# Kernel tuning notes

Measured on AMD Instinct MI355X. Metric: run time of the kernel, lower is better.

Reference implementation:

```python
import jax, jax.numpy as jnp
import numpy as np

WIN = 7
N = WIN * WIN            # 49 tokens per window
HEADS = 6
C = 192
NW = 4096                # windows per image
B_ = 8192                # batch * num_windows
EPS = 1e-12              # F.normalize eps


def _make_relative_position_index():
    # mirrors the torch buffer construction (torch.meshgrid default = 'ij')
    coords = np.stack(np.meshgrid(np.arange(WIN), np.arange(WIN), indexing='ij'))  # [2,7,7]
    flat = coords.reshape(2, -1)                                # [2,49]
    rel = flat[:, :, None] - flat[:, None, :]                   # [2,49,49]
    rel = rel.transpose(1, 2, 0).astype(np.int64)               # [49,49,2]
    rel[..., 0] += WIN - 1
    rel[..., 1] += WIN - 1
    rel[..., 0] *= 2 * WIN - 1
    return rel.sum(-1)                                          # [49,49], values in [0, 169)


def setup_inputs() -> dict:
    key = jax.random.key(0)
    ks = jax.random.split(key, 8)
    x = jax.random.normal(ks[0], (B_, N, C), dtype=jnp.float32)
    mask = jnp.zeros((NW, N, N), dtype=jnp.float32)
    d_l = jax.random.uniform(ks[1], (B_,), dtype=jnp.float32)
    w = 0.02
    Wq = jax.random.normal(ks[2], (C, C), dtype=jnp.float32) * w
    Wk = jax.random.normal(ks[3], (C, C), dtype=jnp.float32) * w
    Wv = jax.random.normal(ks[4], (C, C), dtype=jnp.float32) * w
    Wp = jax.random.normal(ks[5], (C, C), dtype=jnp.float32) * w
    temperature = jnp.ones((HEADS, 1, 1), dtype=jnp.float32)
    rpb_table = jax.random.normal(ks[6], ((2 * WIN - 1) ** 2, HEADS), dtype=jnp.float32) * w
    rel_index = jnp.asarray(_make_relative_position_index(), dtype=jnp.int32)
    return {"x": x, "mask": mask, "d_l": d_l, "Wq": Wq, "Wk": Wk, "Wv": Wv,
            "Wp": Wp, "temperature": temperature, "rpb_table": rpb_table,
            "rel_index": rel_index}


def _l2norm(t):
    # F.normalize(dim=-1): t / max(||t||_2, eps)
    n = jnp.sqrt(jnp.sum(t * t, axis=-1, keepdims=True))
    return t / jnp.maximum(n, EPS)


def reference(x, mask, d_l, Wq, Wk, Wv, Wp, temperature, rpb_table, rel_index):
    b, n, c = x.shape
    hd = c // HEADS  # head dim = 32

    def split_heads(t):
        return t.reshape(b, n, HEADS, hd).transpose(0, 2, 1, 3)  # b h n d

    q = split_heads(x @ Wq.T)
    k = split_heads(x @ Wk.T)
    v = split_heads(x @ Wv.T)

    q = _l2norm(q)
    k = _l2norm(k)

    attn = jnp.einsum('bhnd,bhmd->bhnm', q, k) * temperature  # temperature [h,1,1] broadcasts

    bias = rpb_table[rel_index.reshape(-1)].reshape(n, n, HEADS)  # gather [49,49,h]
    attn = attn + bias.transpose(2, 0, 1)[None]                   # [1,h,n,n]

    nW = mask.shape[0]
    attn = attn.reshape(b // nW, nW, HEADS, n, n) + mask[None, :, None]
    attn = attn.reshape(b, HEADS, n, n)

    attn = attn * d_l[:, None, None, None]  # degrade-level modulation
    attn = jax.nn.softmax(attn, axis=-1)

    out = jnp.einsum('bhnm,bhmd->bhnd', attn, v)
    out = out.transpose(0, 2, 1, 3).reshape(b, n, c)
    return out @ Wp.T
```

## Files before the change

### kernel.cpp

```cpp
#include <hip/hip_runtime.h>

#define NTOK 49
#define HEADS 6
#define CDIM 192
#define NWIN 4096

typedef unsigned short u16;
typedef unsigned int u32;
typedef unsigned long long u64;
typedef __attribute__((ext_vector_type(8))) __bf16 bf16x8;
typedef __attribute__((ext_vector_type(4))) float floatx4;

#define OFF_X 0
#define OFF_Q 25600
#define OFF_K 51200
#define OFF_V 76800
#define OFF_P 104448
#define LDS_BYTES 122880

__device__ __forceinline__ u16 f2bf(float f) {
  union { float f; u32 u; } v; v.f = f;
  u32 u = v.u;
  u = (u + 0x7FFFu + ((u >> 16) & 1u)) >> 16;
  return (u16)u;
}
__device__ __forceinline__ float bf2f(u16 u) {
  union { u32 u; float f; } v; v.u = ((u32)u) << 16;
  return v.f;
}
__device__ __forceinline__ void st4bf(u16* p, float a, float b, float c, float d) {
  u64 t = (u64)f2bf(a) | ((u64)f2bf(b) << 16) | ((u64)f2bf(c) << 32) | ((u64)f2bf(d) << 48);
  *(u64*)p = t;
}

__global__ __launch_bounds__(256)
void wprep(const float* __restrict__ Wq, const float* __restrict__ Wk,
           const float* __restrict__ Wv, const float* __restrict__ Wp,
           const float* __restrict__ rpb, const int* __restrict__ rel,
           u16* __restrict__ w_bf, float* __restrict__ bias) {
  const int tid = blockIdx.x * blockDim.x + threadIdx.x;
  const int stride = gridDim.x * blockDim.x;
  for (int i = tid; i < 4 * CDIM * CDIM; i += stride) {
    const int p = i / (CDIM * CDIM), e = i % (CDIM * CDIM);
    float v = (p == 0) ? Wq[e] : (p == 1) ? Wk[e] : (p == 2) ? Wv[e] : Wp[e];
    w_bf[i] = f2bf(v);
  }
  for (int i = tid; i < HEADS * NTOK * NTOK; i += stride) {
    const int h = i / (NTOK * NTOK), nm = i % (NTOK * NTOK);
    bias[i] = rpb[rel[nm] * HEADS + h];
  }
}

__global__ __launch_bounds__(512, 2)
void wattn_main(const float* __restrict__ x, const float* __restrict__ mask,
                const float* __restrict__ d_l, const float* __restrict__ temp,
                const u16* __restrict__ w_bf, const float* __restrict__ bias,
                float* __restrict__ out) {
  extern __shared__ __align__(16) char smem[];
  u16* Xb = (u16*)(smem + OFF_X);
  u16* Qn = (u16*)(smem + OFF_Q);
  u16* Kn = (u16*)(smem + OFF_K);
  u16* Vt = (u16*)(smem + OFF_V);
  u16* Pw = (u16*)(smem + OFF_P);

  const int b = blockIdx.x;
  const int tid = threadIdx.x;
  const int wave = tid >> 6;
  const int lane = tid & 63;
  const int g = lane >> 4;
  const int nl = lane & 15;

  {
    const float* xb = x + (size_t)b * (NTOK * CDIM);
    for (int i = tid; i < NTOK * CDIM / 4; i += 512) {
      const int n = i / 48;
      const int c = (i - n * 48) * 4;
      const float4 v = *(const float4*)(xb + n * CDIM + c);
      st4bf(Xb + n * 200 + c, v.x, v.y, v.z, v.w);
    }
    for (int i = tid; i < 15 * 48; i += 512) {
      const int n = 49 + i / 48;
      const int c = (i % 48) * 4;
      *(u64*)(Xb + n * 200 + c) = 0ull;
    }
  }
  __syncthreads();

  {
    bf16x8 xf[4][6];
#pragma unroll
    for (int nt = 0; nt < 4; ++nt)
#pragma unroll
      for (int k = 0; k < 6; ++k)
        xf[nt][k] = *(const bf16x8*)(Xb + (nt * 16 + nl) * 200 + k * 32 + g * 8);

    for (int u = wave; u < 36; u += 8) {
      const int p = u / 12, o = u % 12;
      const u16* wb = w_bf + p * (CDIM * CDIM) + (o * 16 + nl) * CDIM + g * 8;
      bf16x8 wf[6];
#pragma unroll
      for (int k = 0; k < 6; ++k) wf[k] = *(const bf16x8*)(wb + k * 32);
      floatx4 acc[4];
#pragma unroll
      for (int nt = 0; nt < 4; ++nt) acc[nt] = (floatx4){0.f, 0.f, 0.f, 0.f};
      if (p < 2) {
#pragma unroll
        for (int k = 0; k < 6; ++k)
#pragma unroll
          for (int nt = 0; nt < 4; ++nt)
            acc[nt] = __builtin_amdgcn_mfma_f32_16x16x32_bf16(wf[k], xf[nt][k], acc[nt], 0, 0, 0);
        u16* dst = (p == 0 ? Qn : Kn);
#pragma unroll
        for (int nt = 0; nt < 4; ++nt)
          st4bf(dst + (nt * 16 + nl) * 200 + o * 16 + g * 4,
                acc[nt][0], acc[nt][1], acc[nt][2], acc[nt][3]);
      } else {
#pragma unroll
        for (int k = 0; k < 6; ++k)
#pragma unroll
          for (int nt = 0; nt < 4; ++nt)
            acc[nt] = __builtin_amdgcn_mfma_f32_16x16x32_bf16(xf[nt][k], wf[k], acc[nt], 0, 0, 0);
#pragma unroll
        for (int nt = 0; nt < 4; ++nt)
          st4bf(Vt + (o * 16 + nl) * 72 + nt * 16 + g * 4,
                acc[nt][0], acc[nt][1], acc[nt][2], acc[nt][3]);
      }
    }
  }
  __syncthreads();

  {
    const int sub = tid & 3;
    for (int ru = tid >> 2; ru < 2 * HEADS * NTOK; ru += 128) {
      const int t = ru / (HEADS * NTOK);
      const int rem = ru - t * (HEADS * NTOK);
      const int h = rem / NTOK, n = rem - h * NTOK;
      u16* base = (t == 0 ? Qn : Kn) + n * 200 + h * 32 + sub * 8;
      u64 lo = *(u64*)base;
      u64 hi = *(u64*)(base + 4);
      float f[8];
#pragma unroll
      for (int e = 0; e < 4; ++e) f[e] = bf2f((u16)(lo >> (16 * e)));
#pragma unroll
      for (int e = 0; e < 4; ++e) f[4 + e] = bf2f((u16)(hi >> (16 * e)));
      float ss = 0.f;
#pragma unroll
      for (int e = 0; e < 8; ++e) ss += f[e] * f[e];
      ss += __shfl_xor(ss, 1);
      ss += __shfl_xor(ss, 2);
      const float inv = 1.0f / fmaxf(sqrtf(ss), 1e-12f);
      st4bf(base, f[0] * inv, f[1] * inv, f[2] * inv, f[3] * inv);
      st4bf(base + 4, f[4] * inv, f[5] * inv, f[6] * inv, f[7] * inv);
    }
  }
  __syncthreads();

  {
    const float dl = d_l[b];
    const int wmask = b & (NWIN - 1);
    u16* Pb = Pw + wave * (16 * 72);
    for (int t = wave; t < 24; t += 8) {
      const int h = t >> 2, nt2 = t & 3;
      const int n = nt2 * 16 + nl;
      const int ncl = n < 49 ? n : 48;
      const float tdl = temp[h] * dl;
      const bf16x8 qf = *(const bf16x8*)(Qn + n * 200 + h * 32 + g * 8);
      floatx4 sacc[4];
#pragma unroll
      for (int rt = 0; rt < 4; ++rt) {
        const bf16x8 kf = *(const bf16x8*)(Kn + (rt * 16 + nl) * 200 + h * 32 + g * 8);
        sacc[rt] = __builtin_amdgcn_mfma_f32_16x16x32_bf16(kf, qf, (floatx4){0.f, 0.f, 0.f, 0.f}, 0, 0, 0);
      }
      const float* brow = bias + (h * NTOK + ncl) * NTOK;
      const float* mrow = mask + ((size_t)wmask * NTOK + ncl) * NTOK;
      float L[4][4];
      float pmax = -1e30f;
#pragma unroll
      for (int rt = 0; rt < 4; ++rt)
#pragma unroll
        for (int r = 0; r < 4; ++r) {
          const int m = rt * 16 + g * 4 + r;
          const int mcl = m < 49 ? m : 48;
          const float bm = (brow[mcl] + mrow[mcl]) * dl;
          float lv = fmaf(sacc[rt][r], tdl, bm);
          lv = (m < 49) ? lv : -1e30f;
          L[rt][r] = lv;
          pmax = fmaxf(pmax, lv);
        }
      pmax = fmaxf(pmax, __shfl_xor(pmax, 16));
      pmax = fmaxf(pmax, __shfl_xor(pmax, 32));
      float psum = 0.f;
#pragma unroll
      for (int rt = 0; rt < 4; ++rt)
#pragma unroll
        for (int r = 0; r < 4; ++r) {
          const int m = rt * 16 + g * 4 + r;
          const float e = (m < 49) ? __expf(L[rt][r] - pmax) : 0.f;
          L[rt][r] = e;
          psum += e;
        }
      psum += __shfl_xor(psum, 16);
      psum += __shfl_xor(psum, 32);
      const float rinv = 1.0f / psum;
#pragma unroll
      for (int rt = 0; rt < 4; ++rt)
        st4bf(Pb + nl * 72 + rt * 16 + g * 4,
              L[rt][0] * rinv, L[rt][1] * rinv, L[rt][2] * rinv, L[rt][3] * rinv);
      floatx4 oacc[2];
      oacc[0] = (floatx4){0.f, 0.f, 0.f, 0.f};
      oacc[1] = (floatx4){0.f, 0.f, 0.f, 0.f};
#pragma unroll
      for (int ks = 0; ks < 2; ++ks) {
        const bf16x8 pf = *(const bf16x8*)(Pb + nl * 72 + ks * 32 + g * 8);
#pragma unroll
        for (int dt = 0; dt < 2; ++dt) {
          const bf16x8 vf = *(const bf16x8*)(Vt + (h * 32 + dt * 16 + nl) * 72 + ks * 32 + g * 8);
          oacc[dt] = __builtin_amdgcn_mfma_f32_16x16x32_bf16(vf, pf, oacc[dt], 0, 0, 0);
        }
      }
#pragma unroll
      for (int dt = 0; dt < 2; ++dt)
        st4bf(Xb + n * 200 + h * 32 + dt * 16 + g * 4,
              oacc[dt][0], oacc[dt][1], oacc[dt][2], oacc[dt][3]);
    }
  }
  __syncthreads();

  {
    bf16x8 af[4][6];
#pragma unroll
    for (int nt = 0; nt < 4; ++nt)
#pragma unroll
      for (int k = 0; k < 6; ++k)
        af[nt][k] = *(const bf16x8*)(Xb + (nt * 16 + nl) * 200 + k * 32 + g * 8);
    float* outb = out + (size_t)b * (NTOK * CDIM);
    const u16* wpb = w_bf + 3 * (CDIM * CDIM);
    for (int o = wave; o < 12; o += 8) {
      const u16* wb = wpb + (o * 16 + nl) * CDIM + g * 8;
      bf16x8 wf[6];
#pragma unroll
      for (int k = 0; k < 6; ++k) wf[k] = *(const bf16x8*)(wb + k * 32);
      floatx4 acc[4];
#pragma unroll
      for (int nt = 0; nt < 4; ++nt) acc[nt] = (floatx4){0.f, 0.f, 0.f, 0.f};
#pragma unroll
      for (int k = 0; k < 6; ++k)
#pragma unroll
        for (int nt = 0; nt < 4; ++nt)
          acc[nt] = __builtin_amdgcn_mfma_f32_16x16x32_bf16(wf[k], af[nt][k], acc[nt], 0, 0, 0);
#pragma unroll
      for (int nt = 0; nt < 4; ++nt) {
        const int n = nt * 16 + nl;
        if (n < 49) {
          float4 v;
          v.x = acc[nt][0]; v.y = acc[nt][1]; v.z = acc[nt][2]; v.w = acc[nt][3];
          *(float4*)(outb + n * CDIM + o * 16 + g * 4) = v;
        }
      }
    }
  }
}

extern "C" void kernel_launch(void* const* d_in, const int* in_sizes, int n_in,
                              void* d_out, int out_size, void* d_ws, size_t ws_size,
                              hipStream_t stream) {
  const float* x    = (const float*)d_in[0];
  const float* mask = (const float*)d_in[1];
  const float* dl   = (const float*)d_in[2];
  const float* Wq   = (const float*)d_in[3];
  const float* Wk   = (const float*)d_in[4];
  const float* Wv   = (const float*)d_in[5];
  const float* Wp   = (const float*)d_in[6];
  const float* temp = (const float*)d_in[7];
  const float* rpb  = (const float*)d_in[8];
  const int*   rel  = (const int*)d_in[9];

  u16* w_bf = (u16*)d_ws;
  float* bias = (float*)((char*)d_ws + (size_t)4 * CDIM * CDIM * sizeof(u16));
  float* o = (float*)d_out;

  (void)hipFuncSetAttribute((const void*)wattn_main,
                            hipFuncAttributeMaxDynamicSharedMemorySize, LDS_BYTES);

  wprep<<<256, 256, 0, stream>>>(Wq, Wk, Wv, Wp, rpb, rel, w_bf, bias);
  wattn_main<<<8192, 512, LDS_BYTES, stream>>>(x, mask, dl, temp, w_bf, bias, o);
}
```

Before: 646.9 us.

## Shrink LDS footprint via buffer aliasing and register-resident P to raise occupancy

The change reduces LDS from about 120KB to 75KB by aliasing X with V^T and Q with the attention output. It keeps softmax probabilities in registers, using cross-lane shuffles instead of an LDS round trip, and swizzles the V^T layout to avoid bank conflicts. The QKV projection is split so each wave pair handles half the tokens, and the output projection is re-tiled. Launch bounds go to 4 blocks per CU so more windows are resident. In exchange it adds an extra barrier, more shuffles, register pressure from the 4-block bound, and scalar (uncoalesced) final output stores.

Result: slower. 841.2 us (+30.0%).

```diff
diff --git a/kernel.cpp b/kernel.cpp
--- a/kernel.cpp
+++ b/kernel.cpp
@@ -10,13 +10,14 @@
 typedef unsigned long long u64;
 typedef __attribute__((ext_vector_type(8))) __bf16 bf16x8;
 typedef __attribute__((ext_vector_type(4))) float floatx4;
-
-#define OFF_X 0
-#define OFF_Q 25600
-#define OFF_K 51200
-#define OFF_V 76800
-#define OFF_P 104448
-#define LDS_BYTES 122880
+typedef __attribute__((ext_vector_type(4))) u32 u32x4;
+
+struct __attribute__((aligned(4))) F4 { float f[4]; };
+
+#define R1_OFF 0
+#define R2_OFF 25600
+#define R3_OFF 51200
+#define LDS_BYTES 76800
 
 __device__ __forceinline__ u16 f2bf(float f) {
   union { float f; u32 u; } v; v.f = f;
@@ -24,13 +25,20 @@
   u = (u + 0x7FFFu + ((u >> 16) & 1u)) >> 16;
   return (u16)u;
 }
+__device__ __forceinline__ void st4bf(u16* p, float a, float b, float c, float d) {
+  u64 t = (u64)f2bf(a) | ((u64)f2bf(b) << 16) | ((u64)f2bf(c) << 32) | ((u64)f2bf(d) << 48);
+  *(u64*)p = t;
+}
 __device__ __forceinline__ float bf2f(u16 u) {
   union { u32 u; float f; } v; v.u = ((u32)u) << 16;
   return v.f;
 }
-__device__ __forceinline__ void st4bf(u16* p, float a, float b, float c, float d) {
-  u64 t = (u64)f2bf(a) | ((u64)f2bf(b) << 16) | ((u64)f2bf(c) << 32) | ((u64)f2bf(d) << 48);
-  *(u64*)p = t;
+__device__ __forceinline__ u32 pack2bf(float lo, float hi) {
+  return (u32)f2bf(lo) | ((u32)f2bf(hi) << 16);
+}
+__device__ __forceinline__ bf16x8 frag_from_words(u32 a, u32 b, u32 c, u32 d) {
+  u32x4 t = {a, b, c, d};
+  return __builtin_bit_cast(bf16x8, t);
 }
 
 __global__ __launch_bounds__(256)
@@ -51,17 +59,17 @@
   }
 }
 
-__global__ __launch_bounds__(512, 2)
+__global__ __launch_bounds__(512, 4)
 void wattn_main(const float* __restrict__ x, const float* __restrict__ mask,
                 const float* __restrict__ d_l, const float* __restrict__ temp,
                 const u16* __restrict__ w_bf, const float* __restrict__ bias,
                 float* __restrict__ out) {
   extern __shared__ __align__(16) char smem[];
-  u16* Xb = (u16*)(smem + OFF_X);
-  u16* Qn = (u16*)(smem + OFF_Q);
-  u16* Kn = (u16*)(smem + OFF_K);
-  u16* Vt = (u16*)(smem + OFF_V);
-  u16* Pw = (u16*)(smem + OFF_P);
+  u16* Xs  = (u16*)(smem + R1_OFF);
+  u16* Vt  = (u16*)(smem + R1_OFF);
+  u16* Qn  = (u16*)(smem + R2_OFF);
+  u16* AOB = (u16*)(smem + R2_OFF);
+  u16* Kn  = (u16*)(smem + R3_OFF);
 
   const int b = blockIdx.x;
   const int tid = threadIdx.x;
@@ -72,58 +80,62 @@
 
   {
     const float* xb = x + (size_t)b * (NTOK * CDIM);
-    for (int i = tid; i < NTOK * CDIM / 4; i += 512) {
+    for (int i = tid; i < NTOK * 48; i += 512) {
       const int n = i / 48;
       const int c = (i - n * 48) * 4;
       const float4 v = *(const float4*)(xb + n * CDIM + c);
-      st4bf(Xb + n * 200 + c, v.x, v.y, v.z, v.w);
+      st4bf(Xs + n * 200 + c, v.x, v.y, v.z, v.w);
     }
     for (int i = tid; i < 15 * 48; i += 512) {
-      const int n = 49 + i / 48;
+      const int n = NTOK + i / 48;
       const int c = (i % 48) * 4;
-      *(u64*)(Xb + n * 200 + c) = 0ull;
-    }
-  }
-  __syncthreads();
-
-  {
-    bf16x8 xf[4][6];
-#pragma unroll
-    for (int nt = 0; nt < 4; ++nt)
+      *(u64*)(Xs + n * 200 + c) = 0ull;
+    }
+  }
+  __syncthreads();
+
+  const int nthalf = wave & 1;
+  const int wg = wave >> 1;
+  bf16x8 xf[2][6];
+#pragma unroll
+  for (int nt2 = 0; nt2 < 2; ++nt2)
+#pragma unroll
+    for (int k = 0; k < 6; ++k)
+      xf[nt2][k] = *(const bf16x8*)(Xs + (nthalf * 32 + nt2 * 16 + nl) * 200 + k * 32 + g * 8);
+  __syncthreads();
+
+  for (int t = wg; t < 36; t += 4) {
+    const int p = t / 12, o = t % 12;
+    const u16* wb = w_bf + p * (CDIM * CDIM) + (o * 16 + nl) * CDIM + g * 8;
+    bf16x8 wf[6];
+#pragma unroll
+    for (int k = 0; k < 6; ++k) wf[k] = *(const bf16x8*)(wb + k * 32);
+    floatx4 acc[2];
+    acc[0] = (floatx4){0.f, 0.f, 0.f, 0.f};
+    acc[1] = (floatx4){0.f, 0.f, 0.f, 0.f};
+    if (p < 2) {
 #pragma unroll
       for (int k = 0; k < 6; ++k)
-        xf[nt][k] = *(const bf16x8*)(Xb + (nt * 16 + nl) * 200 + k * 32 + g * 8);
-
-    for (int u = wave; u < 36; u += 8) {
-      const int p = u / 12, o = u % 12;
-      const u16* wb = w_bf + p * (CDIM * CDIM) + (o * 16 + nl) * CDIM + g * 8;
-      bf16x8 wf[6];
-#pragma unroll
-      for (int k = 0; k < 6; ++k) wf[k] = *(const bf16x8*)(wb + k * 32);
-      floatx4 acc[4];
-#pragma unroll
-      for (int nt = 0; nt < 4; ++nt) acc[nt] = (floatx4){0.f, 0.f, 0.f, 0.f};
-      if (p < 2) {
-#pragma unroll
-        for (int k = 0; k < 6; ++k)
-#pragma unroll
-          for (int nt = 0; nt < 4; ++nt)
-            acc[nt] = __builtin_amdgcn_mfma_f32_16x16x32_bf16(wf[k], xf[nt][k], acc[nt], 0, 0, 0);
-        u16* dst = (p == 0 ? Qn : Kn);
-#pragma unroll
-        for (int nt = 0; nt < 4; ++nt)
-          st4bf(dst + (nt * 16 + nl) * 200 + o * 16 + g * 4,
-                acc[nt][0], acc[nt][1], acc[nt][2], acc[nt][3]);
-      } else {
-#pragma unroll
-        for (int k = 0; k < 6; ++k)
-#pragma unroll
-          for (int nt = 0; nt < 4; ++nt)
-            acc[nt] = __builtin_amdgcn_mfma_f32_16x16x32_bf16(xf[nt][k], wf[k], acc[nt], 0, 0, 0);
-#pragma unroll
-        for (int nt = 0; nt < 4; ++nt)
-          st4bf(Vt + (o * 16 + nl) * 72 + nt * 16 + g * 4,
-                acc[nt][0], acc[nt][1], acc[nt][2], acc[nt][3]);
+#pragma unroll
+        for (int nt2 = 0; nt2 < 2; ++nt2)
+          acc[nt2] = __builtin_amdgcn_mfma_f32_16x16x32_bf16(wf[k], xf[nt2][k], acc[nt2], 0, 0, 0);
+      u16* dst = (p == 0 ? Qn : Kn);
+#pragma unroll
+      for (int nt2 = 0; nt2 < 2; ++nt2)
+        st4bf(dst + (nthalf * 32 + nt2 * 16 + nl) * 200 + o * 16 + g * 4,
+              acc[nt2][0], acc[nt2][1], acc[nt2][2], acc[nt2][3]);
+    } else {
+#pragma unroll
+      for (int k = 0; k < 6; ++k)
+#pragma unroll
+        for (int nt2 = 0; nt2 < 2; ++nt2)
+          acc[nt2] = __builtin_amdgcn_mfma_f32_16x16x32_bf16(xf[nt2][k], wf[k], acc[nt2], 0, 0, 0);
+      const int row = o * 16 + nl;
+#pragma unroll
+      for (int nt2 = 0; nt2 < 2; ++nt2) {
+        const int col = nthalf * 32 + nt2 * 16 + g * 4;
+        const int colS = (col + ((nl & 3) << 4)) & 63;
+        st4bf(Vt + row * 64 + colS, acc[nt2][0], acc[nt2][1], acc[nt2][2], acc[nt2][3]);
       }
     }
   }
@@ -155,107 +167,138 @@
   }
   __syncthreads();
 
+  const float dl = d_l[b];
+  const int wmask = b & (NWIN - 1);
+  const int srcA = nl + ((lane & 16) << 1);
+  const int srcB = srcA + 16;
+  const bool hi = (g >> 1) != 0;
+  u32 pf[3][2][4];
+#pragma unroll
+  for (int i = 0; i < 3; ++i) {
+    const int t = wave + 8 * i;
+    const int h = t >> 2, nt = t & 3;
+    const int n = nt * 16 + nl;
+    const int ncl = n < NTOK ? n : NTOK - 1;
+    const float tdl = temp[h] * dl;
+    const bf16x8 qf = *(const bf16x8*)(Qn + n * 200 + h * 32 + g * 8);
+    floatx4 sacc[4];
+#pragma unroll
+    for (int rt = 0; rt < 4; ++rt) {
+      const bf16x8 kf = *(const bf16x8*)(Kn + (rt * 16 + nl) * 200 + h * 32 + g * 8);
+      sacc[rt] = __builtin_amdgcn_mfma_f32_16x16x32_bf16(kf, qf, (floatx4){0.f, 0.f, 0.f, 0.f}, 0, 0, 0);
+    }
+    const float* brow = bias + (h * NTOK + ncl) * NTOK;
+    const float* mrow = mask + ((size_t)wmask * NTOK + ncl) * NTOK;
+    float L[4][4];
+    float pmax = -1e30f;
+#pragma unroll
+    for (int rt = 0; rt < 3; ++rt) {
+      const F4 b4 = *(const F4*)(brow + rt * 16 + g * 4);
+      const F4 m4 = *(const F4*)(mrow + rt * 16 + g * 4);
+#pragma unroll
+      for (int r = 0; r < 4; ++r) {
+        const float lv = fmaf(sacc[rt][r], tdl, (b4.f[r] + m4.f[r]) * dl);
+        L[rt][r] = lv;
+        pmax = fmaxf(pmax, lv);
+      }
+    }
+    {
+      const float lv48 = fmaf(sacc[3][0], tdl, (brow[48] + mrow[48]) * dl);
+#pragma unroll
+      for (int r = 0; r < 4; ++r) L[3][r] = -1e30f;
+      if (g == 0) { L[3][0] = lv48; pmax = fmaxf(pmax, lv48); }
+    }
+    pmax = fmaxf(pmax, __shfl_xor(pmax, 16));
+    pmax = fmaxf(pmax, __shfl_xor(pmax, 32));
+    float psum = 0.f;
+#pragma unroll
+    for (int rt = 0; rt < 4; ++rt)
+#pragma unroll
+      for (int r = 0; r < 4; ++r) {
+        const float e = __expf(L[rt][r] - pmax);
+        L[rt][r] = e;
+        psum += e;
+      }
+    psum += __shfl_xor(psum, 16);
+    psum += __shfl_xor(psum, 32);
+    const float rinv = 1.0f / psum;
+    u32 pk[4][2];
+#pragma unroll
+    for (int rt = 0; rt < 4; ++rt)
+#pragma unroll
+      for (int w2 = 0; w2 < 2; ++w2)
+        pk[rt][w2] = pack2bf(L[rt][2 * w2] * rinv, L[rt][2 * w2 + 1] * rinv);
+#pragma unroll
+    for (int ks = 0; ks < 2; ++ks) {
+      const u32 a0 = __shfl((int)pk[2 * ks][0], srcA), b0 = __shfl((int)pk[2 * ks + 1][0], srcA);
+      const u32 a1 = __shfl((int)pk[2 * ks][1], srcA), b1 = __shfl((int)pk[2 * ks + 1][1], srcA);
+      const u32 a2 = __shfl((int)pk[2 * ks][0], srcB), b2 = __shfl((int)pk[2 * ks + 1][0], srcB);
+      const u32 a3 = __shfl((int)pk[2 * ks][1], srcB), b3 = __shfl((int)pk[2 * ks + 1][1], srcB);
+      pf[i][ks][0] = hi ? b0 : a0;
+      pf[i][ks][1] = hi ? b1 : a1;
+      pf[i][ks][2] = hi ? b2 : a2;
+      pf[i][ks][3] = hi ? b3 : a3;
+    }
+  }
+  __syncthreads();
+
+#pragma unroll
+  for (int i = 0; i < 3; ++i) {
+    const int t = wave + 8 * i;
+    const int h = t >> 2, nt = t & 3;
+    floatx4 oacc[2];
+    oacc[0] = (floatx4){0.f, 0.f, 0.f, 0.f};
+    oacc[1] = (floatx4){0.f, 0.f, 0.f, 0.f};
+#pragma unroll
+    for (int ks = 0; ks < 2; ++ks) {
+      const bf16x8 pfr = frag_from_words(pf[i][ks][0], pf[i][ks][1], pf[i][ks][2], pf[i][ks][3]);
+#pragma unroll
+      for (int dt = 0; dt < 2; ++dt) {
+        const int row = h * 32 + dt * 16 + nl;
+        const int colS = (ks * 32 + g * 8 + ((nl & 3) << 4)) & 63;
+        const bf16x8 vf = *(const bf16x8*)(Vt + row * 64 + colS);
+        oacc[dt] = __builtin_amdgcn_mfma_f32_16x16x32_bf16(vf, pfr, oacc[dt], 0, 0, 0);
+      }
+    }
+    u32 pka[2][2];
+#pragma unroll
+    for (int dt = 0; dt < 2; ++dt)
+#pragma unroll
+      for (int w2 = 0; w2 < 2; ++w2)
+        pka[dt][w2] = pack2bf(oacc[dt][2 * w2], oacc[dt][2 * w2 + 1]);
+    const u32 a0 = __shfl((int)pka[0][0], srcA), b0 = __shfl((int)pka[1][0], srcA);
+    const u32 a1 = __shfl((int)pka[0][1], srcA), b1 = __shfl((int)pka[1][1], srcA);
+    const u32 a2 = __shfl((int)pka[0][0], srcB), b2 = __shfl((int)pka[1][0], srcB);
+    const u32 a3 = __shfl((int)pka[0][1], srcB), b3 = __shfl((int)pka[1][1], srcB);
+    u32x4 frag;
+    frag[0] = hi ? b0 : a0;
+    frag[1] = hi ? b1 : a1;
+    frag[2] = hi ? b2 : a2;
+    frag[3] = hi ? b3 : a3;
+    *(u32x4*)(AOB + ((size_t)(nt * 6 + h) * 64 + lane) * 8) = frag;
+  }
+  __syncthreads();
+
   {
-    const float dl = d_l[b];
-    const int wmask = b & (NWIN - 1);
-    u16* Pb = Pw + wave * (16 * 72);
-    for (int t = wave; t < 24; t += 8) {
-      const int h = t >> 2, nt2 = t & 3;
-      const int n = nt2 * 16 + nl;
-      const int ncl = n < 49 ? n : 48;
-      const float tdl = temp[h] * dl;
-      const bf16x8 qf = *(const bf16x8*)(Qn + n * 200 + h * 32 + g * 8);
-      floatx4 sacc[4];
-#pragma unroll
-      for (int rt = 0; rt < 4; ++rt) {
-        const bf16x8 kf = *(const bf16x8*)(Kn + (rt * 16 + nl) * 200 + h * 32 + g * 8);
-        sacc[rt] = __builtin_amdgcn_mfma_f32_16x16x32_bf16(kf, qf, (floatx4){0.f, 0.f, 0.f, 0.f}, 0, 0, 0);
-      }
-      const float* brow = bias + (h * NTOK + ncl) * NTOK;
-      const float* mrow = mask + ((size_t)wmask * NTOK + ncl) * NTOK;
-      float L[4][4];
-      float pmax = -1e30f;
-#pragma unroll
-      for (int rt = 0; rt < 4; ++rt)
-#pragma unroll
-        for (int r = 0; r < 4; ++r) {
-          const int m = rt * 16 + g * 4 + r;
-          const int mcl = m < 49 ? m : 48;
-          const float bm = (brow[mcl] + mrow[mcl]) * dl;
-          float lv = fmaf(sacc[rt][r], tdl, bm);
-          lv = (m < 49) ? lv : -1e30f;
-          L[rt][r] = lv;
-          pmax = fmaxf(pmax, lv);
-        }
-      pmax = fmaxf(pmax, __shfl_xor(pmax, 16));
-      pmax = fmaxf(pmax, __shfl_xor(pmax, 32));
-      float psum = 0.f;
-#pragma unroll
-      for (int rt = 0; rt < 4; ++rt)
-#pragma unroll
-        for (int r = 0; r < 4; ++r) {
-          const int m = rt * 16 + g * 4 + r;
-          const float e = (m < 49) ? __expf(L[rt][r] - pmax) : 0.f;
-          L[rt][r] = e;
-          psum += e;
-        }
-      psum += __shfl_xor(psum, 16);
-      psum += __shfl_xor(psum, 32);
-      const float rinv = 1.0f / psum;
-#pragma unroll
-      for (int rt = 0; rt < 4; ++rt)
-        st4bf(Pb + nl * 72 + rt * 16 + g * 4,
-              L[rt][0] * rinv, L[rt][1] * rinv, L[rt][2] * rinv, L[rt][3] * rinv);
-      floatx4 oacc[2];
-      oacc[0] = (floatx4){0.f, 0.f, 0.f, 0.f};
-      oacc[1] = (floatx4){0.f, 0.f, 0.f, 0.f};
-#pragma unroll
-      for (int ks = 0; ks < 2; ++ks) {
-        const bf16x8 pf = *(const bf16x8*)(Pb + nl * 72 + ks * 32 + g * 8);
-#pragma unroll
-        for (int dt = 0; dt < 2; ++dt) {
-          const bf16x8 vf = *(const bf16x8*)(Vt + (h * 32 + dt * 16 + nl) * 72 + ks * 32 + g * 8);
-          oacc[dt] = __builtin_amdgcn_mfma_f32_16x16x32_bf16(vf, pf, oacc[dt], 0, 0, 0);
-        }
-      }
-#pragma unroll
-      for (int dt = 0; dt < 2; ++dt)
-        st4bf(Xb + n * 200 + h * 32 + dt * 16 + g * 4,
-              oacc[dt][0], oacc[dt][1], oacc[dt][2], oacc[dt][3]);
-    }
-  }
-  __syncthreads();
-
-  {
-    bf16x8 af[4][6];
-#pragma unroll
-    for (int nt = 0; nt < 4; ++nt)
-#pragma unroll
-      for (int k = 0; k < 6; ++k)
-        af[nt][k] = *(const bf16x8*)(Xb + (nt * 16 + nl) * 200 + k * 32 + g * 8);
     float* outb = out + (size_t)b * (NTOK * CDIM);
     const u16* wpb = w_bf + 3 * (CDIM * CDIM);
-    for (int o = wave; o < 12; o += 8) {
-      const u16* wb = wpb + (o * 16 + nl) * CDIM + g * 8;
-      bf16x8 wf[6];
-#pragma unroll
-      for (int k = 0; k < 6; ++k) wf[k] = *(const bf16x8*)(wb + k * 32);
-      floatx4 acc[4];
-#pragma unroll
-      for (int nt = 0; nt < 4; ++nt) acc[nt] = (floatx4){0.f, 0.f, 0.f, 0.f};
-#pragma unroll
-      for (int k = 0; k < 6; ++k)
-#pragma unroll
-        for (int nt = 0; nt < 4; ++nt)
-          acc[nt] = __builtin_amdgcn_mfma_f32_16x16x32_bf16(wf[k], af[nt][k], acc[nt], 0, 0, 0);
-#pragma unroll
-      for (int nt = 0; nt < 4; ++nt) {
-        const int n = nt * 16 + nl;
-        if (n < 49) {
-          float4 v;
-          v.x = acc[nt][0]; v.y = acc[nt][1]; v.z = acc[nt][2]; v.w = acc[nt][3];
-          *(float4*)(outb + n * CDIM + o * 16 + g * 4) = v;
-        }
+    for (int t = wave; t < 48; t += 8) {
+      const int o = t >> 2, nt = t & 3;
+      bf16x8 af[6], wfp[6];
+#pragma unroll
+      for (int h = 0; h < 6; ++h)
+        af[h] = *(const bf16x8*)(AOB + ((nt * 6 + h) * 64 + lane) * 8);
+#pragma unroll
+      for (int ks = 0; ks < 6; ++ks)
+        wfp[ks] = *(const bf16x8*)(wpb + (o * 16 + nl) * CDIM + ks * 32 + g * 8);
+      floatx4 acc = (floatx4){0.f, 0.f, 0.f, 0.f};
+#pragma unroll
+      for (int ks = 0; ks < 6; ++ks)
+        acc = __builtin_amdgcn_mfma_f32_16x16x32_bf16(af[ks], wfp[ks], acc, 0, 0, 0);
+#pragma unroll
+      for (int r = 0; r < 4; ++r) {
+        const int tok = nt * 16 + g * 4 + r;
+        if (tok < NTOK) outb[tok * CDIM + o * 16 + nl] = acc[r];
       }
     }
   }
```

## Split fused window attention into QKV-projection and attention kernels via workspace

Applied to the files above, without the earlier changes.

Replaces the single large-LDS fused kernel with two kernels. The first projects Q, K and V into bf16 global buffers, keeping x fragments in registers. The second does the normalization, softmax, PV and output projection using small LDS, so more blocks fit per CU. This aims to remove the occupancy limit from 120KB of LDS, but costs a global round trip of about 150MB of intermediates. If the workspace is too small it falls back to the old fused kernel.

Result: slower. 1.004 ms (+55.2%).

```diff
diff --git a/kernel.cpp b/kernel.cpp
--- a/kernel.cpp
+++ b/kernel.cpp
@@ -10,13 +10,9 @@
 typedef unsigned long long u64;
 typedef __attribute__((ext_vector_type(8))) __bf16 bf16x8;
 typedef __attribute__((ext_vector_type(4))) float floatx4;
-
-#define OFF_X 0
-#define OFF_Q 25600
-#define OFF_K 51200
-#define OFF_V 76800
-#define OFF_P 104448
-#define LDS_BYTES 122880
+typedef __attribute__((ext_vector_type(4))) u32 u32x4;
+
+struct __attribute__((aligned(4))) F4 { float f[4]; };
 
 __device__ __forceinline__ u16 f2bf(float f) {
   union { float f; u32 u; } v; v.f = f;
@@ -24,13 +20,24 @@
   u = (u + 0x7FFFu + ((u >> 16) & 1u)) >> 16;
   return (u16)u;
 }
+__device__ __forceinline__ void st4bf(u16* p, float a, float b, float c, float d) {
+  u64 t = (u64)f2bf(a) | ((u64)f2bf(b) << 16) | ((u64)f2bf(c) << 32) | ((u64)f2bf(d) << 48);
+  *(u64*)p = t;
+}
 __device__ __forceinline__ float bf2f(u16 u) {
   union { u32 u; float f; } v; v.u = ((u32)u) << 16;
   return v.f;
 }
-__device__ __forceinline__ void st4bf(u16* p, float a, float b, float c, float d) {
-  u64 t = (u64)f2bf(a) | ((u64)f2bf(b) << 16) | ((u64)f2bf(c) << 32) | ((u64)f2bf(d) << 48);
-  *(u64*)p = t;
+__device__ __forceinline__ float bflo(u32 u) {
+  union { u32 u; float f; } v; v.u = u << 16;
+  return v.f;
+}
+__device__ __forceinline__ float bfhi(u32 u) {
+  union { u32 u; float f; } v; v.u = u & 0xffff0000u;
+  return v.f;
+}
+__device__ __forceinline__ u32 pack2bf(float lo, float hi) {
+  return (u32)f2bf(lo) | ((u32)f2bf(hi) << 16);
 }
 
 __global__ __launch_bounds__(256)
@@ -51,17 +58,230 @@
   }
 }
 
+__global__ __launch_bounds__(256, 3)
+void k1_qkv(const float* __restrict__ x, const u16* __restrict__ w_bf,
+            u16* __restrict__ Qg, u16* __restrict__ Kg, u16* __restrict__ Vt) {
+  const int w = blockIdx.x;
+  const int wave = threadIdx.x >> 6;
+  const int lane = threadIdx.x & 63;
+  const int g = lane >> 4, nl = lane & 15;
+  const float* xw = x + (size_t)w * (NTOK * CDIM);
+
+  bf16x8 xf[4][6];
+#pragma unroll
+  for (int nt = 0; nt < 4; ++nt) {
+    const int tok = nt * 16 + nl;
+#pragma unroll
+    for (int k = 0; k < 6; ++k) {
+      if (tok < NTOK) {
+        const float4 lo = *(const float4*)(xw + tok * CDIM + k * 32 + g * 8);
+        const float4 hi = *(const float4*)(xw + tok * CDIM + k * 32 + g * 8 + 4);
+        u32x4 t;
+        t[0] = pack2bf(lo.x, lo.y); t[1] = pack2bf(lo.z, lo.w);
+        t[2] = pack2bf(hi.x, hi.y); t[3] = pack2bf(hi.z, hi.w);
+        xf[nt][k] = __builtin_bit_cast(bf16x8, t);
+      } else {
+        u32x4 t = {0u, 0u, 0u, 0u};
+        xf[nt][k] = __builtin_bit_cast(bf16x8, t);
+      }
+    }
+  }
+
+  for (int t = wave; t < 36; t += 4) {
+    const int p = t / 12, c = t % 12;
+    const u16* wb = w_bf + p * (CDIM * CDIM) + (c * 16 + nl) * CDIM + g * 8;
+    bf16x8 wf[6];
+#pragma unroll
+    for (int k = 0; k < 6; ++k) wf[k] = *(const bf16x8*)(wb + k * 32);
+    floatx4 acc[4];
+#pragma unroll
+    for (int nt = 0; nt < 4; ++nt) acc[nt] = (floatx4){0.f, 0.f, 0.f, 0.f};
+    if (p < 2) {
+#pragma unroll
+      for (int k = 0; k < 6; ++k)
+#pragma unroll
+        for (int nt = 0; nt < 4; ++nt)
+          acc[nt] = __builtin_amdgcn_mfma_f32_16x16x32_bf16(wf[k], xf[nt][k], acc[nt], 0, 0, 0);
+      const int h = c >> 1, half = c & 1;
+      u16* dst = (p == 0 ? Qg : Kg) + (size_t)(w * 6 + h) * (NTOK * 32);
+#pragma unroll
+      for (int nt = 0; nt < 4; ++nt) {
+        const int tok = nt * 16 + nl;
+        if (tok < NTOK)
+          st4bf(dst + tok * 32 + half * 16 + g * 4,
+                acc[nt][0], acc[nt][1], acc[nt][2], acc[nt][3]);
+      }
+    } else {
+#pragma unroll
+      for (int k = 0; k < 6; ++k)
+#pragma unroll
+        for (int nt = 0; nt < 4; ++nt)
+          acc[nt] = __builtin_amdgcn_mfma_f32_16x16x32_bf16(xf[nt][k], wf[k], acc[nt], 0, 0, 0);
+      u16* dst = Vt + ((size_t)w * CDIM + c * 16 + nl) * 64;
+#pragma unroll
+      for (int nt = 0; nt < 4; ++nt)
+        st4bf(dst + nt * 16 + g * 4, acc[nt][0], acc[nt][1], acc[nt][2], acc[nt][3]);
+    }
+  }
+}
+
+#define K2_LDS (25600 + 13824 + 3072)
+__global__ __launch_bounds__(384, 4)
+void k2_attn(const u16* __restrict__ Qg, const u16* __restrict__ Kg,
+             const u16* __restrict__ Vt, const float* __restrict__ mask,
+             const float* __restrict__ d_l, const float* __restrict__ temp,
+             const float* __restrict__ bias, const u16* __restrict__ w_bf,
+             float* __restrict__ out) {
+  extern __shared__ __align__(16) char smem[];
+  u16* AO = (u16*)smem;
+  u16* Pall = (u16*)(smem + 25600);
+  float* nrm = (float*)(smem + 25600 + 13824);
+
+  const int w = blockIdx.x;
+  const int h = threadIdx.x >> 6;
+  const int lane = threadIdx.x & 63;
+  const int g = lane >> 4, nl = lane & 15;
+  const float dl = d_l[w];
+  const float tdl = temp[h] * dl;
+  const size_t qkbase = (size_t)(w * 6 + h) * (NTOK * 32);
+
+  {
+    const u16* krow = Kg + qkbase + lane * 32;
+    const u16* qrow = Qg + qkbase + lane * 32;
+    float ssk = 0.f, ssq = 0.f;
+#pragma unroll
+    for (int q4 = 0; q4 < 4; ++q4) {
+      const u32x4 kk = *(const u32x4*)(krow + q4 * 8);
+      const u32x4 qq = *(const u32x4*)(qrow + q4 * 8);
+#pragma unroll
+      for (int e = 0; e < 4; ++e) {
+        const float k0 = bflo(kk[e]), k1 = bfhi(kk[e]);
+        const float q0 = bflo(qq[e]), q1 = bfhi(qq[e]);
+        ssk = fmaf(k0, k0, fmaf(k1, k1, ssk));
+        ssq = fmaf(q0, q0, fmaf(q1, q1, ssq));
+      }
+    }
+    nrm[h * 128 + lane] = 1.f / fmaxf(sqrtf(ssk), 1e-12f);
+    nrm[h * 128 + 64 + lane] = 1.f / fmaxf(sqrtf(ssq), 1e-12f);
+  }
+
+  u16* Pb = Pall + h * (16 * 72);
+  bf16x8 kf[4];
+#pragma unroll
+  for (int rt = 0; rt < 4; ++rt)
+    kf[rt] = *(const bf16x8*)(Kg + qkbase + (rt * 16 + nl) * 32 + g * 8);
+  const int wm = w & (NWIN - 1);
+
+  for (int nt = 0; nt < 4; ++nt) {
+    const int n = nt * 16 + nl;
+    const int ncl = n < NTOK ? n : NTOK - 1;
+    const bf16x8 qf = *(const bf16x8*)(Qg + qkbase + n * 32 + g * 8);
+    floatx4 sacc[4];
+#pragma unroll
+    for (int rt = 0; rt < 4; ++rt)
+      sacc[rt] = __builtin_amdgcn_mfma_f32_16x16x32_bf16(kf[rt], qf, (floatx4){0.f, 0.f, 0.f, 0.f}, 0, 0, 0);
+    const float qr = nrm[h * 128 + 64 + n] * tdl;
+    const float* brow = bias + (h * NTOK + ncl) * NTOK;
+    const float* mrow = mask + ((size_t)wm * NTOK + ncl) * NTOK;
+    float L[4][4];
+    float pmax = -1e30f;
+#pragma unroll
+    for (int rt = 0; rt < 3; ++rt) {
+      const F4 b4 = *(const F4*)(brow + rt * 16 + g * 4);
+      const F4 m4 = *(const F4*)(mrow + rt * 16 + g * 4);
+      const F4 kr = *(const F4*)(nrm + h * 128 + rt * 16 + g * 4);
+#pragma unroll
+      for (int r = 0; r < 4; ++r) {
+        const float lv = fmaf(sacc[rt][r] * kr.f[r], qr, (b4.f[r] + m4.f[r]) * dl);
+        L[rt][r] = lv;
+        pmax = fmaxf(pmax, lv);
+      }
+    }
+    {
+      const float lv48 = fmaf(sacc[3][0] * nrm[h * 128 + 48], qr, (brow[48] + mrow[48]) * dl);
+      L[3][0] = L[3][1] = L[3][2] = L[3][3] = -1e30f;
+      if (g == 0) { L[3][0] = lv48; pmax = fmaxf(pmax, lv48); }
+    }
+    pmax = fmaxf(pmax, __shfl_xor(pmax, 16));
+    pmax = fmaxf(pmax, __shfl_xor(pmax, 32));
+    float psum = 0.f;
+#pragma unroll
+    for (int rt = 0; rt < 4; ++rt)
+#pragma unroll
+      for (int r = 0; r < 4; ++r) {
+        const float e = __expf(L[rt][r] - pmax);
+        L[rt][r] = e;
+        psum += e;
+      }
+    psum += __shfl_xor(psum, 16);
+    psum += __shfl_xor(psum, 32);
+    const float rinv = 1.0f / psum;
+#pragma unroll
+    for (int rt = 0; rt < 4; ++rt)
+      st4bf(Pb + nl * 72 + rt * 16 + g * 4,
+            L[rt][0] * rinv, L[rt][1] * rinv, L[rt][2] * rinv, L[rt][3] * rinv);
+    floatx4 oacc[2];
+    oacc[0] = (floatx4){0.f, 0.f, 0.f, 0.f};
+    oacc[1] = (floatx4){0.f, 0.f, 0.f, 0.f};
+#pragma unroll
+    for (int ks = 0; ks < 2; ++ks) {
+      const bf16x8 pfr = *(const bf16x8*)(Pb + nl * 72 + ks * 32 + g * 8);
+#pragma unroll
+      for (int dt = 0; dt < 2; ++dt) {
+        const bf16x8 vf = *(const bf16x8*)(Vt + ((size_t)w * CDIM + h * 32 + dt * 16 + nl) * 64 + ks * 32 + g * 8);
+        oacc[dt] = __builtin_amdgcn_mfma_f32_16x16x32_bf16(vf, pfr, oacc[dt], 0, 0, 0);
+      }
+    }
+#pragma unroll
+    for (int dt = 0; dt < 2; ++dt)
+      st4bf(AO + n * 200 + h * 32 + dt * 16 + g * 4,
+            oacc[dt][0], oacc[dt][1], oacc[dt][2], oacc[dt][3]);
+  }
+  __syncthreads();
+
+  {
+    float* outb = out + (size_t)w * (NTOK * CDIM);
+    const u16* wpb = w_bf + 3 * (CDIM * CDIM);
+    for (int t = h; t < 48; t += 6) {
+      const int o = t >> 2, nt = t & 3;
+      bf16x8 af[6], wfp[6];
+#pragma unroll
+      for (int k = 0; k < 6; ++k)
+        af[k] = *(const bf16x8*)(AO + (nt * 16 + nl) * 200 + k * 32 + g * 8);
+#pragma unroll
+      for (int k = 0; k < 6; ++k)
+        wfp[k] = *(const bf16x8*)(wpb + (o * 16 + nl) * CDIM + k * 32 + g * 8);
+      floatx4 acc = (floatx4){0.f, 0.f, 0.f, 0.f};
+#pragma unroll
+      for (int k = 0; k < 6; ++k)
+        acc = __builtin_amdgcn_mfma_f32_16x16x32_bf16(af[k], wfp[k], acc, 0, 0, 0);
+#pragma unroll
+      for (int r = 0; r < 4; ++r) {
+        const int tok = nt * 16 + g * 4 + r;
+        if (tok < NTOK) outb[tok * CDIM + o * 16 + nl] = acc[r];
+      }
+    }
+  }
+}
+
+#define FB_OFF_X 0
+#define FB_OFF_Q 25600
+#define FB_OFF_K 51200
+#define FB_OFF_V 76800
+#define FB_OFF_P 104448
+#define FB_LDS_BYTES 122880
+
 __global__ __launch_bounds__(512, 2)
-void wattn_main(const float* __restrict__ x, const float* __restrict__ mask,
-                const float* __restrict__ d_l, const float* __restrict__ temp,
-                const u16* __restrict__ w_bf, const float* __restrict__ bias,
-                float* __restrict__ out) {
+void wattn_fused(const float* __restrict__ x, const float* __restrict__ mask,
+                 const float* __restrict__ d_l, const float* __restrict__ temp,
+                 const u16* __restrict__ w_bf, const float* __restrict__ bias,
+                 float* __restrict__ out) {
   extern __shared__ __align__(16) char smem[];
-  u16* Xb = (u16*)(smem + OFF_X);
-  u16* Qn = (u16*)(smem + OFF_Q);
-  u16* Kn = (u16*)(smem + OFF_K);
-  u16* Vt = (u16*)(smem + OFF_V);
-  u16* Pw = (u16*)(smem + OFF_P);
+  u16* Xb = (u16*)(smem + FB_OFF_X);
+  u16* Qn = (u16*)(smem + FB_OFF_Q);
+  u16* Kn = (u16*)(smem + FB_OFF_K);
+  u16* Vt = (u16*)(smem + FB_OFF_V);
+  u16* Pw = (u16*)(smem + FB_OFF_P);
 
   const int b = blockIdx.x;
   const int tid = threadIdx.x;
@@ -274,14 +494,30 @@
   const float* temp = (const float*)d_in[7];
   const float* rpb  = (const float*)d_in[8];
   const int*   rel  = (const int*)d_in[9];
+  float* o = (float*)d_out;
+
+  const size_t off_bias = 294912;
+  const size_t off_q = 352768;
+  const size_t sz_qk = (size_t)8192 * 6 * NTOK * 32 * 2 + 4096;
+  const size_t off_k = off_q + sz_qk;
+  const size_t off_v = off_k + sz_qk;
+  const size_t sz_v = (size_t)8192 * CDIM * 64 * 2;
+  const size_t need = off_v + sz_v;
 
   u16* w_bf = (u16*)d_ws;
-  float* bias = (float*)((char*)d_ws + (size_t)4 * CDIM * CDIM * sizeof(u16));
-  float* o = (float*)d_out;
-
-  (void)hipFuncSetAttribute((const void*)wattn_main,
-                            hipFuncAttributeMaxDynamicSharedMemorySize, LDS_BYTES);
+  float* bias = (float*)((char*)d_ws + off_bias);
 
   wprep<<<256, 256, 0, stream>>>(Wq, Wk, Wv, Wp, rpb, rel, w_bf, bias);
-  wattn_main<<<8192, 512, LDS_BYTES, stream>>>(x, mask, dl, temp, w_bf, bias, o);
-}
+
+  if (ws_size >= need) {
+    u16* Qg = (u16*)((char*)d_ws + off_q);
+    u16* Kg = (u16*)((char*)d_ws + off_k);
+    u16* Vt = (u16*)((char*)d_ws + off_v);
+    k1_qkv<<<8192, 256, 0, stream>>>(x, w_bf, Qg, Kg, Vt);
+    k2_attn<<<8192, 384, K2_LDS, stream>>>(Qg, Kg, Vt, mask, dl, temp, bias, w_bf, o);
+  } else {
+    (void)hipFuncSetAttribute((const void*)wattn_fused,
+                              hipFuncAttributeMaxDynamicSharedMemorySize, FB_LDS_BYTES);
+    wattn_fused<<<8192, 512, FB_LDS_BYTES, stream>>>(x, mask, dl, temp, w_bf, bias, o);
+  }
+}
```
